# Kernel optimization log

Hardware: AMD Instinct MI355X
Metric: run time of the kernel (lower is better)

## Reference

```python
import jax, jax.numpy as jnp
import numpy as np

H = 16  # num_heads


def setup_inputs() -> dict:
    key = jax.random.key(0)
    ks = jax.random.split(key, 8)
    B, N, C = 16, 4096, 512
    hd = C // H
    sc = lambda k, shape: jax.random.normal(k, shape, jnp.float32) * 0.02
    return {
        "x": jax.random.normal(ks[0], (B, N, C), jnp.float32),
        "Wqkv": sc(ks[1], (C, 3 * C)),
        "bqkv": sc(ks[2], (3 * C,)),
        "pos_enc": jnp.zeros((1, N, C), jnp.float32),
        "dwc_w": sc(ks[3], (hd, 1, 5, 5)),  # OIHW, depthwise: groups = hd
        "dwc_b": sc(ks[4], (hd,)),
        "Wproj": sc(ks[5], (C, C)),
        "bproj": sc(ks[6], (C,)),
    }


def reference(x, Wqkv, bqkv, pos_enc, dwc_w, dwc_b, Wproj, bproj):
    B, N, C = x.shape
    hd = C // H
    # qkv projection
    qkv = x @ Wqkv + bqkv                       # (B, N, 3C)
    q, k, v = jnp.split(qkv, 3, axis=-1)
    k = k + pos_enc
    q = jax.nn.relu(q)
    k = jax.nn.relu(k)

    def heads(t):  # (B, N, C) -> (B*H, N, hd), fp32 as in the torch autocast-off block
        return t.reshape(B, N, H, hd).transpose(0, 2, 1, 3).reshape(B * H, N, hd).astype(jnp.float32)

    q, k, v = heads(q), heads(k), heads(v)
    # normalization z_i = 1 / (q_i . sum_j k_j + eps)
    z = 1.0 / (jnp.einsum('bic,bc->bi', q, k.sum(axis=1)) + 1e-6)   # (B*H, N)
    # kv-first path: i*j*(c+d) > c*d*(i+j) for N=4096, hd=32
    kv = jnp.einsum('bjc,bjd->bcd', k, v)                           # (B*H, hd, hd)
    out = jnp.einsum('bic,bcd->bid', q, kv) * z[..., None]          # (B*H, N, hd)
    # depthwise 5x5 conv on v reshaped to a square feature map
    w = int(N ** 0.5)
    fm = v.transpose(0, 2, 1).reshape(B * H, hd, w, w)
    fm = jax.lax.conv_general_dilated(
        fm, dwc_w, window_strides=(1, 1), padding=[(2, 2), (2, 2)],
        dimension_numbers=('NCHW', 'OIHW', 'NCHW'), feature_group_count=hd)
    fm = fm + dwc_b[None, :, None, None]
    fm = fm.reshape(B * H, hd, N).transpose(0, 2, 1)
    out = out + fm
    # merge heads and project
    out = out.reshape(B, H, N, hd).transpose(0, 2, 1, 3).reshape(B, N, C)
    return out @ Wproj + bproj
```

## Files before the change

### kernel.cpp

```cpp
#include <hip/hip_runtime.h>
#include <stdint.h>

typedef short bf16x8 __attribute__((ext_vector_type(8)));
typedef float f32x4 __attribute__((ext_vector_type(4)));
typedef unsigned short u16x8 __attribute__((ext_vector_type(8)));

__device__ __forceinline__ unsigned short f2bf(float f){
  uint32_t u = __builtin_bit_cast(uint32_t, f);
  u += 0x7FFFu + ((u >> 16) & 1u);
  return (unsigned short)(u >> 16);
}
__device__ __forceinline__ float bf2f(unsigned short h){
  uint32_t u = ((uint32_t)h) << 16;
  return __builtin_bit_cast(float, u);
}
__device__ __forceinline__ float bflo(uint32_t dw){
  return __builtin_bit_cast(float, dw << 16);
}
__device__ __forceinline__ float bfhi(uint32_t dw){
  return __builtin_bit_cast(float, dw & 0xffff0000u);
}

__device__ __forceinline__ void gload_lds16(const void* g, void* l){
  __builtin_amdgcn_global_load_lds(
      (const __attribute__((address_space(1))) uint32_t*)(g),
      (__attribute__((address_space(3))) uint32_t*)(l),
      16, 0, 0);
}

__global__ __launch_bounds__(256) void convert_x_k(const float* __restrict__ x,
                                                   unsigned short* __restrict__ xb){
  size_t i = (size_t)blockIdx.x * 256 + threadIdx.x;
  const float4* p = (const float4*)x + i * 2;
  float4 a = p[0], b = p[1];
  u16x8 o;
  o[0] = f2bf(a.x); o[1] = f2bf(a.y); o[2] = f2bf(a.z); o[3] = f2bf(a.w);
  o[4] = f2bf(b.x); o[5] = f2bf(b.y); o[6] = f2bf(b.z); o[7] = f2bf(b.w);
  *(u16x8*)(xb + i * 8) = o;
}

__global__ __launch_bounds__(256) void transpose_w_k(const float* __restrict__ Wqkv,
                                                     const float* __restrict__ Wproj,
                                                     unsigned short* __restrict__ Wqkvt,
                                                     unsigned short* __restrict__ Wprojt){
  __shared__ unsigned short t[64][68];
  int bid = blockIdx.x;
  const float* src; unsigned short* dst; int c0, j0, sstride, dstride;
  if (bid < 192){
    src = Wqkv;  dst = Wqkvt;  sstride = 1536; dstride = 512;
    c0 = (bid / 24) * 64;  j0 = (bid % 24) * 64;
  } else {
    int e = bid - 192;
    src = Wproj; dst = Wprojt; sstride = 512;  dstride = 512;
    c0 = (e >> 3) * 64;    j0 = (e & 7) * 64;
  }
  int tid = threadIdx.x;
  int rl = tid >> 6;
  int cl = tid & 63;
  #pragma unroll
  for (int i = 0; i < 16; ++i){
    int cr = i * 4 + rl;
    t[cl][cr] = f2bf(src[(size_t)(c0 + cr) * sstride + j0 + cl]);
  }
  __syncthreads();
  #pragma unroll
  for (int i = 0; i < 16; ++i){
    int jr = i * 4 + rl;
    dst[(size_t)(j0 + jr) * dstride + c0 + cl] = t[jr][cl];
  }
}

__global__ __launch_bounds__(512, 2) void gemm_qkv(
    const unsigned short* __restrict__ A,
    const unsigned short* __restrict__ Bt,
    const float* __restrict__ bias,
    const float* __restrict__ pos_enc,
    unsigned short* __restrict__ oq,
    unsigned short* __restrict__ ok,
    unsigned short* __restrict__ ov,
    int NTN)
{
  __shared__ unsigned short As[256 * 64];
  __shared__ unsigned short Bs[128 * 64];
  int tid = threadIdx.x, lane = tid & 63, wid = tid >> 6;
  int nwg = gridDim.x;
  int b0 = blockIdx.x;
  int cpx = nwg >> 3;
  int swz = (b0 & 7) * cpx + (b0 >> 3);
  int tm = swz / NTN, tn = swz - tm * NTN;
  int row0 = tm << 8, col0 = tn << 7;
  int wr = wid >> 1, wc = wid & 1;

  f32x4 acc[4][4];
  #pragma unroll
  for (int m = 0; m < 4; ++m)
    #pragma unroll
    for (int n = 0; n < 4; ++n)
      acc[m][n] = (f32x4){0.f, 0.f, 0.f, 0.f};

  for (int kt = 0; kt < 8; ++kt){
    int k0 = kt * 64;
    #pragma unroll
    for (int it = 0; it < 4; ++it){
      int c = it * 512 + tid;
      int r = c >> 3;
      int scs = ((c & 7) ^ (r & 7)) * 8;
      gload_lds16(A + (size_t)(row0 + r) * 512 + k0 + scs, &As[c * 8]);
    }
    #pragma unroll
    for (int it = 0; it < 2; ++it){
      int c = it * 512 + tid;
      int r = c >> 3;
      int scs = ((c & 7) ^ (r & 7)) * 8;
      gload_lds16(Bt + (size_t)(col0 + r) * 512 + k0 + scs, &Bs[c * 8]);
    }
    __syncthreads();
    #pragma unroll
    for (int kk = 0; kk < 2; ++kk){
      bf16x8 af[4], bfr[4];
      int kcs = ((kk * 4 + (lane >> 4)) ^ (lane & 7)) * 8;
      #pragma unroll
      for (int m = 0; m < 4; ++m)
        af[m] = *(const bf16x8*)&As[(wr * 64 + m * 16 + (lane & 15)) * 64 + kcs];
      #pragma unroll
      for (int n = 0; n < 4; ++n)
        bfr[n] = *(const bf16x8*)&Bs[(wc * 64 + n * 16 + (lane & 15)) * 64 + kcs];
      #pragma unroll
      for (int m = 0; m < 4; ++m)
        #pragma unroll
        for (int n = 0; n < 4; ++n)
          acc[m][n] = __builtin_amdgcn_mfma_f32_16x16x32_bf16(af[m], bfr[n], acc[m][n], 0, 0, 0);
    }
    __syncthreads();
  }

  int part = col0 >> 9;
  int ccb = (col0 & 511) + wc * 64;
  unsigned short* scr = &As[wid * 2048];
  #pragma unroll
  for (int mh = 0; mh < 2; ++mh){
    #pragma unroll
    for (int mm = 0; mm < 2; ++mm){
      int m = mh * 2 + mm;
      #pragma unroll
      for (int n = 0; n < 4; ++n){
        #pragma unroll
        for (int r = 0; r < 4; ++r){
          int lrow = mm * 16 + (lane >> 4) * 4 + r;
          int lcol = n * 16 + (lane & 15);
          float val = acc[m][n][r] + bias[col0 + wc * 64 + lcol];
          if (part == 0) val = fmaxf(val, 0.f);
          int pch = (lcol >> 3) ^ ((lrow >> 2) & 3);
          scr[lrow * 64 + pch * 8 + (lcol & 7)] = f2bf(val);
        }
      }
    }
    #pragma unroll
    for (int i = 0; i < 4; ++i){
      int idx = i * 64 + lane;
      int r2 = idx >> 3, c2 = idx & 7;
      int pch = c2 ^ ((r2 >> 2) & 3);
      u16x8 vals = *(const u16x8*)&scr[r2 * 64 + pch * 8];
      int grow = row0 + wr * 64 + mh * 32 + r2;
      int bb = grow >> 12, nn = grow & 4095;
      int cc = ccb + c2 * 8;
      int h = cc >> 5, d = cc & 31;
      size_t dst = ((size_t)((bb << 4) + h) * 4096 + nn) * 32 + d;
      if (part == 1){
        const float4* pe = (const float4*)(pos_enc + (size_t)nn * 512 + cc);
        float4 p0 = pe[0], p1 = pe[1];
        u16x8 o;
        o[0] = f2bf(fmaxf(bf2f(vals[0]) + p0.x, 0.f));
        o[1] = f2bf(fmaxf(bf2f(vals[1]) + p0.y, 0.f));
        o[2] = f2bf(fmaxf(bf2f(vals[2]) + p0.z, 0.f));
        o[3] = f2bf(fmaxf(bf2f(vals[3]) + p0.w, 0.f));
        o[4] = f2bf(fmaxf(bf2f(vals[4]) + p1.x, 0.f));
        o[5] = f2bf(fmaxf(bf2f(vals[5]) + p1.y, 0.f));
        o[6] = f2bf(fmaxf(bf2f(vals[6]) + p1.z, 0.f));
        o[7] = f2bf(fmaxf(bf2f(vals[7]) + p1.w, 0.f));
        *(u16x8*)(ok + dst) = o;
      } else if (part == 0){
        *(u16x8*)(oq + dst) = vals;
      } else {
        *(u16x8*)(ov + dst) = vals;
      }
    }
  }
}

__global__ __launch_bounds__(512, 1) void gemm_proj(
    const unsigned short* __restrict__ A,
    const unsigned short* __restrict__ Bt,
    const float* __restrict__ bias,
    float* __restrict__ op,
    int NTN)
{
  __shared__ unsigned short As[2][256 * 64];
  __shared__ unsigned short Bs[2][256 * 64];
  int tid = threadIdx.x, lane = tid & 63, wid = tid >> 6;
  int nwg = gridDim.x;
  int b0 = blockIdx.x;
  int cpx = nwg >> 3;
  int swz = (b0 & 7) * cpx + (b0 >> 3);
  int tm = swz / NTN, tn = swz - tm * NTN;
  int row0 = tm << 8, col0 = tn << 8;
  int wrow = wid >> 2, wcol = wid & 3;

  f32x4 acc[8][4];
  #pragma unroll
  for (int m = 0; m < 8; ++m)
    #pragma unroll
    for (int n = 0; n < 4; ++n)
      acc[m][n] = (f32x4){0.f, 0.f, 0.f, 0.f};

  auto STAGE = [&](int buf, int kt){
    int k0 = kt * 64;
    #pragma unroll
    for (int it = 0; it < 4; ++it){
      int c = it * 512 + tid;
      int r = c >> 3;
      int scs = ((c & 7) ^ (r & 7)) * 8;
      gload_lds16(A + (size_t)(row0 + r) * 512 + k0 + scs, &As[buf][c * 8]);
    }
    #pragma unroll
    for (int it = 0; it < 4; ++it){
      int c = it * 512 + tid;
      int r = c >> 3;
      int scs = ((c & 7) ^ (r & 7)) * 8;
      gload_lds16(Bt + (size_t)(col0 + r) * 512 + k0 + scs, &Bs[buf][c * 8]);
    }
  };
  auto COMPUTE = [&](int buf){
    bf16x8 bfr[4][2];
    #pragma unroll
    for (int kk = 0; kk < 2; ++kk){
      int kcs = ((kk * 4 + (lane >> 4)) ^ (lane & 7)) * 8;
      #pragma unroll
      for (int n = 0; n < 4; ++n)
        bfr[n][kk] = *(const bf16x8*)&Bs[buf][(wcol * 64 + n * 16 + (lane & 15)) * 64 + kcs];
    }
    __builtin_amdgcn_s_setprio(1);
    #pragma unroll
    for (int kk = 0; kk < 2; ++kk){
      int kcs = ((kk * 4 + (lane >> 4)) ^ (lane & 7)) * 8;
      #pragma unroll
      for (int m = 0; m < 8; ++m){
        bf16x8 af = *(const bf16x8*)&As[buf][(wrow * 128 + m * 16 + (lane & 15)) * 64 + kcs];
        #pragma unroll
        for (int n = 0; n < 4; ++n)
          acc[m][n] = __builtin_amdgcn_mfma_f32_16x16x32_bf16(af, bfr[n][kk], acc[m][n], 0, 0, 0);
      }
    }
    __builtin_amdgcn_s_setprio(0);
  };

  STAGE(0, 0);
  STAGE(1, 1);
  #pragma unroll
  for (int t = 0; t < 8; ++t){
    if (t < 7) asm volatile("s_waitcnt vmcnt(8)" ::: "memory");
    else       asm volatile("s_waitcnt vmcnt(0)" ::: "memory");
    __builtin_amdgcn_s_barrier();
    __builtin_amdgcn_sched_barrier(0);
    COMPUTE(t & 1);
    asm volatile("" ::: "memory");
    __builtin_amdgcn_s_barrier();
    if (t + 2 < 8) STAGE(t & 1, t + 2);
  }

  #pragma unroll
  for (int m = 0; m < 8; ++m){
    #pragma unroll
    for (int n = 0; n < 4; ++n){
      #pragma unroll
      for (int r = 0; r < 4; ++r){
        int rrow = row0 + wrow * 128 + m * 16 + (lane >> 4) * 4 + r;
        int ccol = col0 + wcol * 64 + n * 16 + (lane & 15);
        op[(size_t)rrow * 512 + ccol] = acc[m][n][r] + bias[ccol];
      }
    }
  }
}

__global__ __launch_bounds__(256) void kv_k(const unsigned short* __restrict__ kbuf,
                                            const unsigned short* __restrict__ vbuf,
                                            float* __restrict__ kvb,
                                            float* __restrict__ ksb,
                                            uint32_t* __restrict__ vp){
  int bh  = blockIdx.x >> 2;
  int seg = blockIdx.x & 3;
  __shared__ unsigned short ksT[32 * 64];
  __shared__ unsigned short vsT[32 * 64];
  __shared__ float red[4][1024];
  __shared__ float red2[4][32];
  int tid = threadIdx.x, lane = tid & 63, w = tid >> 6;
  const unsigned short* kb = kbuf + (size_t)bh * 131072 + (size_t)seg * 32768;
  const unsigned short* vb = vbuf + (size_t)bh * 131072 + (size_t)seg * 32768;
  uint32_t* vpb = vp + (size_t)bh * 65536 + seg * 1024;

  f32x4 acc00 = (f32x4){0,0,0,0}, acc01 = (f32x4){0,0,0,0};
  f32x4 acc10 = (f32x4){0,0,0,0}, acc11 = (f32x4){0,0,0,0};
  f32x4 ksa0  = (f32x4){0,0,0,0}, ksa1  = (f32x4){0,0,0,0};
  bf16x8 ones;
  #pragma unroll
  for (int j = 0; j < 8; ++j) ones[j] = (short)0x3F80;

  int tok = tid >> 2;
  int ec  = (tid & 3) * 8;

  for (int t = 0; t < 16; ++t){
    __syncthreads();
    u16x8 kk8 = *(const u16x8*)(kb + ((size_t)t * 64 + tok) * 32 + ec);
    u16x8 vv8 = *(const u16x8*)(vb + ((size_t)t * 64 + tok) * 32 + ec);
    #pragma unroll
    for (int j = 0; j < 8; ++j){
      int row = ec + j;
      int sw = (row + (row >> 3)) & 7;
      int col = ((((tok >> 3) ^ sw) << 3) | (tok & 7));
      ksT[row * 64 + col] = kk8[j];
      vsT[row * 64 + col] = vv8[j];
    }
    __syncthreads();
    #pragma unroll
    for (int i = 0; i < 4; ++i){
      int idx = i * 256 + tid;
      int pr = idx >> 6, tk = idx & 63;
      int r0 = pr * 2, r1 = r0 + 1;
      int sw0 = (r0 + (r0 >> 3)) & 7;
      int sw1 = (r1 + (r1 >> 3)) & 7;
      uint32_t lo = vsT[r0 * 64 + ((((tk >> 3) ^ sw0) << 3) | (tk & 7))];
      uint32_t hi = vsT[r1 * 64 + ((((tk >> 3) ^ sw1) << 3) | (tk & 7))];
      vpb[pr * 4096 + t * 64 + tk] = lo | (hi << 16);
    }
    if ((t & 3) == w){
      #pragma unroll
      for (int kk = 0; kk < 2; ++kk){
        int kc = kk * 4 + (lane >> 4);
        int r0 = lane & 15, r1 = 16 + (lane & 15);
        int sw0 = (r0 + (r0 >> 3)) & 7;
        int sw1 = (r1 + (r1 >> 3)) & 7;
        bf16x8 a0 = *(const bf16x8*)&ksT[r0 * 64 + ((kc ^ sw0) << 3)];
        bf16x8 a1 = *(const bf16x8*)&ksT[r1 * 64 + ((kc ^ sw1) << 3)];
        bf16x8 b0 = *(const bf16x8*)&vsT[r0 * 64 + ((kc ^ sw0) << 3)];
        bf16x8 b1 = *(const bf16x8*)&vsT[r1 * 64 + ((kc ^ sw1) << 3)];
        acc00 = __builtin_amdgcn_mfma_f32_16x16x32_bf16(a0, b0, acc00, 0, 0, 0);
        acc01 = __builtin_amdgcn_mfma_f32_16x16x32_bf16(a0, b1, acc01, 0, 0, 0);
        acc10 = __builtin_amdgcn_mfma_f32_16x16x32_bf16(a1, b0, acc10, 0, 0, 0);
        acc11 = __builtin_amdgcn_mfma_f32_16x16x32_bf16(a1, b1, acc11, 0, 0, 0);
        ksa0  = __builtin_amdgcn_mfma_f32_16x16x32_bf16(a0, ones, ksa0, 0, 0, 0);
        ksa1  = __builtin_amdgcn_mfma_f32_16x16x32_bf16(a1, ones, ksa1, 0, 0, 0);
      }
    }
  }
  __syncthreads();
  {
    int q = lane >> 4, c16 = lane & 15;
    #pragma unroll
    for (int r = 0; r < 4; ++r){
      red[w][(q * 4 + r) * 32 + c16]           = acc00[r];
      red[w][(q * 4 + r) * 32 + 16 + c16]      = acc01[r];
      red[w][(16 + q * 4 + r) * 32 + c16]      = acc10[r];
      red[w][(16 + q * 4 + r) * 32 + 16 + c16] = acc11[r];
    }
    if (c16 == 0){
      #pragma unroll
      for (int r = 0; r < 4; ++r){
        red2[w][q * 4 + r]      = ksa0[r];
        red2[w][16 + q * 4 + r] = ksa1[r];
      }
    }
  }
  __syncthreads();
  for (int s = tid; s < 1024; s += 256){
    float sum = red[0][s] + red[1][s] + red[2][s] + red[3][s];
    atomicAdd(&kvb[bh * 1024 + s], sum);
  }
  if (tid < 32){
    atomicAdd(&ksb[bh * 32 + tid],
              red2[0][tid] + red2[1][tid] + red2[2][tid] + red2[3][tid]);
  }
}

__global__ __launch_bounds__(256, 4) void attn_k3(
    const unsigned short* __restrict__ qbuf,
    const uint32_t* __restrict__ vp,
    const float* __restrict__ kvb,
    const float* __restrict__ ksb,
    const float* __restrict__ dwc_w,
    const float* __restrict__ dwc_b,
    unsigned short* __restrict__ attn)
{
  int b0 = blockIdx.x;
  int xcd = b0 & 7, slot = b0 >> 3;
  int bh   = xcd * 32 + (slot >> 3);
  int band = slot & 7;
  int tid = threadIdx.x, lane = tid & 63, w = tid >> 6;
  __shared__ uint32_t outs32[512][18];
  unsigned short* outs = (unsigned short*)outs32;
  __shared__ float zs[512];
  __shared__ float ksum_s[32];

  const unsigned short* qb = qbuf + (size_t)bh * 4096 * 32 + (size_t)band * 512 * 32;
  const uint32_t* vpb = vp + (size_t)bh * 65536;

  if (tid < 32) ksum_s[tid] = ksb[bh * 32 + tid];
  __syncthreads();

  for (int p = 0; p < 2; ++p){
    int t = p * 256 + tid;
    float zd = 0.f;
    #pragma unroll
    for (int pp = 0; pp < 4; ++pp){
      u16x8 qq = *(const u16x8*)(qb + (size_t)t * 32 + pp * 8);
      #pragma unroll
      for (int i = 0; i < 8; ++i) zd += bf2f(qq[i]) * ksum_s[pp * 8 + i];
    }
    zs[t] = 1.f / (zd + 1e-6f);
  }

  bf16x8 bfr[2];
  #pragma unroll
  for (int nc = 0; nc < 2; ++nc){
    bf16x8 t8;
    #pragma unroll
    for (int j = 0; j < 8; ++j){
      int c = (lane >> 4) * 8 + j;
      int d = nc * 16 + (lane & 15);
      t8[j] = (short)f2bf(kvb[bh * 1024 + c * 32 + d]);
    }
    bfr[nc] = t8;
  }
  __syncthreads();

  for (int p = 0; p < 2; ++p){
    f32x4 acc[4][2];
    #pragma unroll
    for (int m = 0; m < 4; ++m){ acc[m][0] = (f32x4){0.f,0.f,0.f,0.f}; acc[m][1] = (f32x4){0.f,0.f,0.f,0.f}; }
    #pragma unroll
    for (int m = 0; m < 4; ++m){
      int row = p * 256 + w * 64 + m * 16 + (lane & 15);
      bf16x8 af = *(const bf16x8*)(qb + (size_t)row * 32 + (lane >> 4) * 8);
      acc[m][0] = __builtin_amdgcn_mfma_f32_16x16x32_bf16(af, bfr[0], acc[m][0], 0, 0, 0);
      acc[m][1] = __builtin_amdgcn_mfma_f32_16x16x32_bf16(af, bfr[1], acc[m][1], 0, 0, 0);
    }
    #pragma unroll
    for (int m = 0; m < 4; ++m)
      #pragma unroll
      for (int nc = 0; nc < 2; ++nc)
        #pragma unroll
        for (int r = 0; r < 4; ++r){
          int lrow = p * 256 + w * 64 + m * 16 + (lane >> 4) * 4 + r;
          int col = nc * 16 + (lane & 15);
          outs[lrow * 36 + col] = f2bf(acc[m][nc][r] * zs[lrow]);
        }
  }
  __syncthreads();

  int x = lane;
  int y0 = band * 8;
  int xm2 = lane - 2, xm1 = lane - 1, xp1 = lane + 1, xp2 = lane + 2;

  for (int pair = 0; pair < 4; ++pair){
    int dbase = w * 8 + pair * 2;
    int pr = w * 4 + pair;
    float w0[25], w1[25];
    #pragma unroll
    for (int j = 0; j < 25; ++j){
      w0[j] = dwc_w[dbase * 25 + j];
      w1[j] = dwc_w[(dbase + 1) * 25 + j];
    }
    float cb0 = dwc_b[dbase], cb1 = dwc_b[dbase + 1];

    uint32_t rowd[12];
    #pragma unroll
    for (int il = 0; il < 12; ++il){
      int yi = y0 - 2 + il;
      rowd[il] = (yi >= 0 && yi < 64)
        ? vpb[pr * 4096 + yi * 64 + x] : 0u;
    }

    float a0[5], a1[5];
    #pragma unroll
    for (int il = 0; il < 12; ++il){
      uint32_t d0 = rowd[il];
      uint32_t dm2 = (uint32_t)__shfl((int)d0, xm2); if (lane < 2)  dm2 = 0;
      uint32_t dm1 = (uint32_t)__shfl((int)d0, xm1); if (lane < 1)  dm1 = 0;
      uint32_t dp1 = (uint32_t)__shfl((int)d0, xp1); if (lane > 62) dp1 = 0;
      uint32_t dp2 = (uint32_t)__shfl((int)d0, xp2); if (lane > 61) dp2 = 0;
      float f0[5], f1[5];
      f0[0] = bflo(dm2); f1[0] = bfhi(dm2);
      f0[1] = bflo(dm1); f1[1] = bfhi(dm1);
      f0[2] = bflo(d0);  f1[2] = bfhi(d0);
      f0[3] = bflo(dp1); f1[3] = bfhi(dp1);
      f0[4] = bflo(dp2); f1[4] = bfhi(dp2);
      #pragma unroll
      for (int ky = 0; ky < 5; ++ky){
        int ol = il - ky;
        if (ol < 0 || ol > 7) continue;
        int s = ol % 5;
        if (ky == 0){
          a0[s] = w0[0] * f0[0];
          a1[s] = w1[0] * f1[0];
          #pragma unroll
          for (int kx = 1; kx < 5; ++kx){
            a0[s] += w0[kx] * f0[kx];
            a1[s] += w1[kx] * f1[kx];
          }
        } else {
          #pragma unroll
          for (int kx = 0; kx < 5; ++kx){
            a0[s] += w0[ky * 5 + kx] * f0[kx];
            a1[s] += w1[ky * 5 + kx] * f1[kx];
          }
        }
      }
      if (il >= 4){
        int ol = il - 4;
        int s = ol % 5;
        int ltok = ol * 64 + x;
        uint32_t ov = outs32[ltok][pr];
        float o0 = bflo(ov) + a0[s] + cb0;
        float o1 = bfhi(ov) + a1[s] + cb1;
        outs32[ltok][pr] = ((uint32_t)f2bf(o1) << 16) | (uint32_t)f2bf(o0);
      }
    }
  }
  __syncthreads();

  int b = bh >> 4, h = bh & 15;
  size_t gbase = ((size_t)b * 4096 + (size_t)band * 512) * 512 + h * 32;
  #pragma unroll
  for (int it = 0; it < 16; ++it){
    int idx = it * 256 + tid;
    int token = idx >> 3, sub = idx & 7;
    uint2 vv = *(const uint2*)&outs32[token][sub * 2];
    *(uint2*)(attn + gbase + (size_t)token * 512 + sub * 4) = vv;
  }
}

extern "C" void kernel_launch(void* const* d_in, const int* in_sizes, int n_in,
                              void* d_out, int out_size, void* d_ws, size_t ws_size,
                              hipStream_t stream) {
  const float* x       = (const float*)d_in[0];
  const float* Wqkv    = (const float*)d_in[1];
  const float* bqkv    = (const float*)d_in[2];
  const float* pos_enc = (const float*)d_in[3];
  const float* dwc_w   = (const float*)d_in[4];
  const float* dwc_b   = (const float*)d_in[5];
  const float* Wproj   = (const float*)d_in[6];
  const float* bproj   = (const float*)d_in[7];
  float* out = (float*)d_out;
  char* ws = (char*)d_ws;

  const size_t off_xb    = 0;
  const size_t off_wqkvt = 67108864;
  const size_t off_wprojt= 68681728;
  const size_t off_q     = 69206016;
  const size_t off_k     = 136314880;
  const size_t off_v     = 203423744;
  const size_t off_kv    = 270532608;
  const size_t off_ksum  = 271581184;
  const size_t needed    = 271613952;
  if (ws_size < needed) return;

  unsigned short* xb     = (unsigned short*)(ws + off_xb);
  unsigned short* wqkvt  = (unsigned short*)(ws + off_wqkvt);
  unsigned short* wprojt = (unsigned short*)(ws + off_wprojt);
  unsigned short* qb     = (unsigned short*)(ws + off_q);
  unsigned short* kb     = (unsigned short*)(ws + off_k);
  unsigned short* vb     = (unsigned short*)(ws + off_v);
  float* kvb = (float*)(ws + off_kv);
  float* ksb = (float*)(ws + off_ksum);
  unsigned short* attn = kb;
  uint32_t* vp = (uint32_t*)(ws + off_xb);

  convert_x_k<<<16384, 256, 0, stream>>>(x, xb);
  transpose_w_k<<<256, 256, 0, stream>>>(Wqkv, Wproj, wqkvt, wprojt);
  gemm_qkv<<<3072, 512, 0, stream>>>(xb, wqkvt, bqkv, pos_enc, qb, kb, vb, 12);
  (void)hipMemsetAsync(kvb, 0, (size_t)(256 * 1024 + 256 * 32) * sizeof(float), stream);
  kv_k<<<1024, 256, 0, stream>>>(kb, vb, kvb, ksb, vp);
  attn_k3<<<2048, 256, 0, stream>>>(qb, vp, kvb, ksb, dwc_w, dwc_b, attn);
  gemm_proj<<<512, 512, 0, stream>>>(attn, wprojt, bproj, out, 2);
}
```

Before: 363.7 us.

## Enlarge QKV GEMM tile to 256x256 with double-buffered LDS prefetch pipeline

Doubles the QKV GEMM output tile width to 256x256 per workgroup (8 waves, each 128x64) and halves the grid. LDS now holds four half-tile slots, so the next k-step's A and B tiles load via global_load_lds while the current step's MFMAs run. Barriers, sched_barrier and setprio interleave loads with compute. In exchange, occupancy drops to one workgroup per CU (launch bounds 512,1), the accumulator register footprint doubles, and more barriers are added per k-step.

```diff
diff --git a/kernel.cpp b/kernel.cpp
--- a/kernel.cpp
+++ b/kernel.cpp
@@ -70,7 +70,7 @@
   }
 }
 
-__global__ __launch_bounds__(512, 2) void gemm_qkv(
+__global__ __launch_bounds__(512, 1) void gemm_qkv(
     const unsigned short* __restrict__ A,
     const unsigned short* __restrict__ Bt,
     const float* __restrict__ bias,
@@ -80,65 +80,107 @@
     unsigned short* __restrict__ ov,
     int NTN)
 {
-  __shared__ unsigned short As[256 * 64];
-  __shared__ unsigned short Bs[128 * 64];
+  __shared__ unsigned short Ar[4][8192];
+  __shared__ unsigned short Br[4][8192];
   int tid = threadIdx.x, lane = tid & 63, wid = tid >> 6;
   int nwg = gridDim.x;
   int b0 = blockIdx.x;
   int cpx = nwg >> 3;
   int swz = (b0 & 7) * cpx + (b0 >> 3);
   int tm = swz / NTN, tn = swz - tm * NTN;
-  int row0 = tm << 8, col0 = tn << 7;
-  int wr = wid >> 1, wc = wid & 1;
-
-  f32x4 acc[4][4];
-  #pragma unroll
-  for (int m = 0; m < 4; ++m)
+  int row0 = tm << 8, col0 = tn << 8;
+  int wrow = wid >> 2, wcol = wid & 3;
+
+  f32x4 acc[8][4];
+  #pragma unroll
+  for (int m = 0; m < 8; ++m)
     #pragma unroll
     for (int n = 0; n < 4; ++n)
       acc[m][n] = (f32x4){0.f, 0.f, 0.f, 0.f};
 
-  for (int kt = 0; kt < 8; ++kt){
-    int k0 = kt * 64;
-    #pragma unroll
-    for (int it = 0; it < 4; ++it){
-      int c = it * 512 + tid;
+  auto STAGE_A = [&](int tt, int h){
+    int slot = (2 * tt + h) & 3;
+    int k0 = tt * 64;
+    #pragma unroll
+    for (int j = 0; j < 2; ++j){
+      int c = j * 512 + tid;
       int r = c >> 3;
       int scs = ((c & 7) ^ (r & 7)) * 8;
-      gload_lds16(A + (size_t)(row0 + r) * 512 + k0 + scs, &As[c * 8]);
-    }
-    #pragma unroll
-    for (int it = 0; it < 2; ++it){
-      int c = it * 512 + tid;
+      gload_lds16(A + (size_t)(row0 + h * 128 + r) * 512 + k0 + scs, &Ar[slot][c * 8]);
+    }
+  };
+  auto STAGE_B = [&](int tt, int h){
+    int slot = (2 * tt + h) & 3;
+    int k0 = tt * 64;
+    #pragma unroll
+    for (int j = 0; j < 2; ++j){
+      int c = j * 512 + tid;
       int r = c >> 3;
       int scs = ((c & 7) ^ (r & 7)) * 8;
-      gload_lds16(Bt + (size_t)(col0 + r) * 512 + k0 + scs, &Bs[c * 8]);
-    }
-    __syncthreads();
-    #pragma unroll
-    for (int kk = 0; kk < 2; ++kk){
-      bf16x8 af[4], bfr[4];
-      int kcs = ((kk * 4 + (lane >> 4)) ^ (lane & 7)) * 8;
-      #pragma unroll
-      for (int m = 0; m < 4; ++m)
-        af[m] = *(const bf16x8*)&As[(wr * 64 + m * 16 + (lane & 15)) * 64 + kcs];
-      #pragma unroll
-      for (int n = 0; n < 4; ++n)
-        bfr[n] = *(const bf16x8*)&Bs[(wc * 64 + n * 16 + (lane & 15)) * 64 + kcs];
-      #pragma unroll
-      for (int m = 0; m < 4; ++m)
+      gload_lds16(Bt + (size_t)(col0 + h * 128 + r) * 512 + k0 + scs, &Br[slot][c * 8]);
+    }
+  };
+
+  STAGE_A(0, 0); STAGE_A(0, 1); STAGE_B(0, 0); STAGE_B(0, 1);
+  asm volatile("s_waitcnt vmcnt(0)" ::: "memory");
+  __builtin_amdgcn_s_barrier();
+  __builtin_amdgcn_sched_barrier(0);
+
+  int crB = (wcol & 1) * 64 + (lane & 15);
+
+  #pragma unroll
+  for (int t = 0; t < 8; ++t){
+    int as = (2 * t + wrow) & 3;
+    int bs = (2 * t + (wcol >> 1)) & 3;
+    bf16x8 bfr[4][2];
+    #pragma unroll
+    for (int p = 0; p < 4; ++p){
+      bf16x8 af[2][2];
+      #pragma unroll
+      for (int kk = 0; kk < 2; ++kk){
+        int kcs = ((kk * 4 + (lane >> 4)) ^ (lane & 7)) * 8;
+        if (p == 0){
+          #pragma unroll
+          for (int n = 0; n < 4; ++n)
+            bfr[n][kk] = *(const bf16x8*)&Br[bs][(crB + n * 16) * 64 + kcs];
+        }
         #pragma unroll
-        for (int n = 0; n < 4; ++n)
-          acc[m][n] = __builtin_amdgcn_mfma_f32_16x16x32_bf16(af[m], bfr[n], acc[m][n], 0, 0, 0);
-    }
-    __syncthreads();
+        for (int mm = 0; mm < 2; ++mm){
+          int ar = (p * 2 + mm) * 16 + (lane & 15);
+          af[mm][kk] = *(const bf16x8*)&Ar[as][ar * 64 + kcs];
+        }
+      }
+      if (t + 1 < 8){
+        if (p == 0){ STAGE_A(t + 1, 0); STAGE_A(t + 1, 1); }
+        else if (p == 1){ STAGE_B(t + 1, 0); STAGE_B(t + 1, 1); }
+      }
+      __builtin_amdgcn_s_barrier();
+      asm volatile("s_waitcnt lgkmcnt(0)" ::: "memory");
+      __builtin_amdgcn_sched_barrier(0);
+      __builtin_amdgcn_s_setprio(1);
+      #pragma unroll
+      for (int kk = 0; kk < 2; ++kk)
+        #pragma unroll
+        for (int mm = 0; mm < 2; ++mm)
+          #pragma unroll
+          for (int n = 0; n < 4; ++n)
+            acc[p * 2 + mm][n] = __builtin_amdgcn_mfma_f32_16x16x32_bf16(
+                af[mm][kk], bfr[n][kk], acc[p * 2 + mm][n], 0, 0, 0);
+      __builtin_amdgcn_s_setprio(0);
+      __builtin_amdgcn_s_barrier();
+    }
+    if (t + 1 < 8){
+      asm volatile("s_waitcnt vmcnt(0)" ::: "memory");
+      __builtin_amdgcn_s_barrier();
+      __builtin_amdgcn_sched_barrier(0);
+    }
   }
 
   int part = col0 >> 9;
-  int ccb = (col0 & 511) + wc * 64;
-  unsigned short* scr = &As[wid * 2048];
-  #pragma unroll
-  for (int mh = 0; mh < 2; ++mh){
+  int ccb = (col0 & 511) + wcol * 64;
+  unsigned short* scr = &Ar[0][0] + wid * 2048;
+  #pragma unroll
+  for (int mh = 0; mh < 4; ++mh){
     #pragma unroll
     for (int mm = 0; mm < 2; ++mm){
       int m = mh * 2 + mm;
@@ -148,7 +190,7 @@
         for (int r = 0; r < 4; ++r){
           int lrow = mm * 16 + (lane >> 4) * 4 + r;
           int lcol = n * 16 + (lane & 15);
-          float val = acc[m][n][r] + bias[col0 + wc * 64 + lcol];
+          float val = acc[m][n][r] + bias[col0 + wcol * 64 + lcol];
           if (part == 0) val = fmaxf(val, 0.f);
           int pch = (lcol >> 3) ^ ((lrow >> 2) & 3);
           scr[lrow * 64 + pch * 8 + (lcol & 7)] = f2bf(val);
@@ -161,7 +203,7 @@
       int r2 = idx >> 3, c2 = idx & 7;
       int pch = c2 ^ ((r2 >> 2) & 3);
       u16x8 vals = *(const u16x8*)&scr[r2 * 64 + pch * 8];
-      int grow = row0 + wr * 64 + mh * 32 + r2;
+      int grow = row0 + wrow * 128 + mh * 32 + r2;
       int bb = grow >> 12, nn = grow & 4095;
       int cc = ccb + c2 * 8;
       int h = cc >> 5, d = cc & 31;
@@ -576,7 +618,7 @@
 
   convert_x_k<<<16384, 256, 0, stream>>>(x, xb);
   transpose_w_k<<<256, 256, 0, stream>>>(Wqkv, Wproj, wqkvt, wprojt);
-  gemm_qkv<<<3072, 512, 0, stream>>>(xb, wqkvt, bqkv, pos_enc, qb, kb, vb, 12);
+  gemm_qkv<<<1536, 512, 0, stream>>>(xb, wqkvt, bqkv, pos_enc, qb, kb, vb, 6);
   (void)hipMemsetAsync(kvb, 0, (size_t)(256 * 1024 + 256 * 32) * sizeof(float), stream);
   kv_k<<<1024, 256, 0, stream>>>(kb, vb, kvb, ksb, vp);
   attn_k3<<<2048, 256, 0, stream>>>(qb, vp, kvb, ksb, dwc_w, dwc_b, attn);
```

New measurement: 369.6 us. Within noise of the previous version (+1.6%).
